# Kernel optimization log

Measured on AMD Instinct MI355X. Metric: run time of the kernel, lower is better.

The kernel has to match this reference:

```python
import jax, jax.numpy as jnp
import numpy as np

N_PITCH, N_DUR, N_TIME, N_VEL = 128, 160, 100, 128
VOCAB = N_PITCH + N_DUR + N_TIME + N_VEL  # 516
B, S = 32, 2048


def _build_vocab_tables():
    # token_type: 0='p', 1='d', 2='t', 3='v'; token_value: numeric suffix of itos_vocab[i]
    tt = np.concatenate([
        np.full(N_PITCH, 0), np.full(N_DUR, 1), np.full(N_TIME, 2), np.full(N_VEL, 3)
    ]).astype(np.int32)
    tv = np.concatenate([
        np.arange(N_PITCH), np.arange(N_DUR), np.arange(N_TIME), np.arange(N_VEL)
    ]).astype(np.float32)
    return jnp.asarray(tt), jnp.asarray(tv)


def setup_inputs() -> dict:
    key = jax.random.key(0)
    k1, k2, k3, k4 = jax.random.split(key, 4)
    token_type, token_value = _build_vocab_tables()
    return {
        "output": jax.random.normal(k1, (B, VOCAB, S), dtype=jnp.float32),
        "target": jax.random.randint(k2, (B, S), 0, VOCAB, dtype=jnp.int32),
        "token_type": token_type,
        "token_value": token_value,
        "coeff": jnp.asarray([0.5, 0.6, 0.2, 0.2], dtype=jnp.float32),
        "harmonic": jnp.asarray([0.6, 0.6, 0.2, 0.2, 0.2, 0.2, 1.5], dtype=jnp.float32),
    }


def _penalty_mask(pred, target, token_type, token_value, coeff, harmonic):
    pt, tt = token_type[pred], token_type[target]      # [B,S] type codes
    pv, tv = token_value[pred], token_value[target]    # [B,S] numeric values
    d = jnp.abs(pv - tv)
    # pitch: harmonic-interval weights (values are integer-valued floats -> exact ==)
    pitch_w = jnp.where(d == 7, harmonic[0],
              jnp.where(d == 5, harmonic[1],
              jnp.where(d == 3, harmonic[2],
              jnp.where(d == 4, harmonic[3],
              jnp.where(d == 1, harmonic[4],
              jnp.where(d == 2, harmonic[5], harmonic[6]))))))
    dur_w = coeff[1] * d / 160.0
    time_w = coeff[2] * d / 100.0
    vel_w = coeff[3] * d / 128.0
    same_type_w = jnp.where(pt == 0, pitch_w,
                  jnp.where(pt == 1, dur_w,
                  jnp.where(pt == 2, time_w, vel_w)))
    return jnp.where(pt != tt, coeff[0], same_type_w)


def reference(output, target, token_type, token_value, coeff, harmonic):
    # Faithful to original: softmax over last (seq) axis, then argmax over vocab axis 1
    sm = jax.nn.softmax(output, axis=-1)
    pred = jnp.argmax(sm, axis=1)                      # [B,S]
    # mean cross-entropy over B*S (class axis = 1)
    logp = jax.nn.log_softmax(output, axis=1)          # [B,V,S]
    nll = -jnp.take_along_axis(logp, target[:, None, :], axis=1)[:, 0, :]
    loss = nll.mean()
    mask = _penalty_mask(pred, target, token_type, token_value, coeff, harmonic)
    high_cost = (loss * mask).mean()
    return loss + high_cost
```

## Files before the change

### kernel.cpp

```cpp
#include <hip/hip_runtime.h>

#define BB 32
#define SS 2048
#define VV 516
#define NBS (BB * SS)
#define NCHUNK 16
#define NPART 256

__device__ inline float waveReduceSum(float v) {
    #pragma unroll
    for (int o = 32; o > 0; o >>= 1) v += __shfl_down(v, o, 64);
    return v;
}

__global__ __launch_bounds__(512, 4) void hl_tile(const float* __restrict__ x,
                                                  const int* __restrict__ target,
                                                  int* __restrict__ ctr,
                                                  float* __restrict__ pSum,
                                                  float* __restrict__ pBest,
                                                  int* __restrict__ pIdx,
                                                  float* __restrict__ xtArr) {
    __shared__ float ldsE[8 * 2048];
    __shared__ float sRcp[8];

    if (blockIdx.x == 0 && threadIdx.x == 0) ctr[0] = 0;

    const int c = blockIdx.x & 15, b = blockIdx.x >> 4;
    const int v0 = 32 * c + (c > 12 ? c - 12 : 0);
    const int nv = (c >= 12) ? 33 : 32;
    const int tid = threadIdx.x, lane = tid & 63, wv = tid >> 6;

    const int s0 = tid << 2;
    const int bs = b * SS + s0;
    int4 tg4 = *(const int4*)(target + bs);
    int tg[4] = {tg4.x, tg4.y, tg4.z, tg4.w};

    float sum[4], best[4], xt[4];
    int bi[4];
    #pragma unroll
    for (int i = 0; i < 4; ++i) { sum[i] = 0.f; best[i] = -1.f; bi[i] = v0; xt[i] = 0.f; }

    const float* xb = x + (size_t)(b * VV + v0) * SS;

    for (int vs = 0; vs < nv; vs += 8) {
        int m = nv - vs; if (m > 8) m = 8;
        if (wv < m) {
            const float* row = xb + (size_t)(vs + wv) * SS;
            float4 v[8];
            #pragma unroll
            for (int j = 0; j < 8; ++j)
                v[j] = *(const float4*)(row + j * 256 + lane * 4);
            float a0 = 0.f, a1 = 0.f, a2 = 0.f, a3 = 0.f;
            #pragma unroll
            for (int j = 0; j < 8; ++j) {
                float4 e;
                e.x = __expf(v[j].x); e.y = __expf(v[j].y);
                e.z = __expf(v[j].z); e.w = __expf(v[j].w);
                *(float4*)(ldsE + wv * 2048 + j * 256 + lane * 4) = e;
                a0 += e.x; a1 += e.y; a2 += e.z; a3 += e.w;
            }
            float ssum = waveReduceSum((a0 + a1) + (a2 + a3));
            if (lane == 0) sRcp[wv] = 1.f / ssum;
        }
        __syncthreads();
        for (int v = 0; v < m; ++v) {
            float r = sRcp[v];
            int vg = v0 + vs + v;
            float4 e4 = *(const float4*)(ldsE + v * 2048 + s0);
            float e[4] = {e4.x, e4.y, e4.z, e4.w};
            #pragma unroll
            for (int i = 0; i < 4; ++i) {
                sum[i] += e[i];
                float sc = e[i] * r;
                if (sc > best[i]) { best[i] = sc; bi[i] = vg; }
            }
        }
        #pragma unroll
        for (int i = 0; i < 4; ++i) {
            int lr = tg[i] - (v0 + vs);
            if (lr >= 0 && lr < m) xt[i] = __logf(ldsE[lr * 2048 + s0 + i]);
        }
        __syncthreads();
    }

    int o = c * NBS + bs;
    *(float4*)(pSum + o)  = make_float4(sum[0], sum[1], sum[2], sum[3]);
    *(float4*)(pBest + o) = make_float4(best[0], best[1], best[2], best[3]);
    *(int4*)(pIdx + o)    = make_int4(bi[0], bi[1], bi[2], bi[3]);
    int v1 = v0 + nv;
    #pragma unroll
    for (int i = 0; i < 4; ++i)
        if (tg[i] >= v0 && tg[i] < v1) xtArr[bs + i] = xt[i];
}

__global__ __launch_bounds__(256) void hl_comb(const int* __restrict__ target,
                                               const int* __restrict__ ttype,
                                               const float* __restrict__ tval,
                                               const float* __restrict__ coeff,
                                               const float* __restrict__ harm,
                                               const float* __restrict__ pSum,
                                               const float* __restrict__ pBest,
                                               const int* __restrict__ pIdx,
                                               const float* __restrict__ xtArr,
                                               float* __restrict__ pNll,
                                               float* __restrict__ pMask,
                                               int* __restrict__ counter,
                                               float* __restrict__ outv) {
    __shared__ float lds[8];
    __shared__ bool isLast;
    int idx = blockIdx.x * 256 + threadIdx.x;

    float sum = 0.f, best = -1e30f;
    int bestIdx = 0;
    #pragma unroll
    for (int c = 0; c < NCHUNK; ++c) {
        int o = c * NBS + idx;
        sum += pSum[o];
        float sc = pBest[o];
        int ii = pIdx[o];
        if (sc > best) { best = sc; bestIdx = ii; }
    }
    int tgt = target[idx];
    float nll = __logf(sum) - xtArr[idx];

    int pt = ttype[bestIdx], tt = ttype[tgt];
    float pv = tval[bestIdx], tv = tval[tgt];
    float d = fabsf(pv - tv);
    float pw = (d == 7.f) ? harm[0] : (d == 5.f) ? harm[1] : (d == 3.f) ? harm[2]
             : (d == 4.f) ? harm[3] : (d == 1.f) ? harm[4] : (d == 2.f) ? harm[5]
             : harm[6];
    float w = (pt == 0) ? pw
            : (pt == 1) ? coeff[1] * d * (1.f / 160.f)
            : (pt == 2) ? coeff[2] * d * (1.f / 100.f)
            :             coeff[3] * d * (1.f / 128.f);
    float mask = (pt != tt) ? coeff[0] : w;

    int lane = threadIdx.x & 63, wvv = threadIdx.x >> 6;
    float rn = waveReduceSum(nll);
    if (lane == 0) lds[wvv] = rn;
    __syncthreads();
    float totN = (threadIdx.x == 0) ? lds[0] + lds[1] + lds[2] + lds[3] : 0.f;
    __syncthreads();
    float rm = waveReduceSum(mask);
    if (lane == 0) lds[wvv] = rm;
    __syncthreads();
    if (threadIdx.x == 0) {
        pNll[blockIdx.x]  = totN;
        pMask[blockIdx.x] = lds[0] + lds[1] + lds[2] + lds[3];
        __threadfence();
        unsigned old = atomicAdd((unsigned*)counter, 1u);
        isLast = (old == NPART - 1);
    }
    __syncthreads();
    if (isLast) {
        __threadfence();
        int t = threadIdx.x;
        float n = waveReduceSum(pNll[t]);
        float m = waveReduceSum(pMask[t]);
        if (lane == 0) { lds[wvv] = n; lds[4 + wvv] = m; }
        __syncthreads();
        if (t == 0) {
            float tn = lds[0] + lds[1] + lds[2] + lds[3];
            float tm = lds[4] + lds[5] + lds[6] + lds[7];
            const float inv = 1.f / (float)NBS;
            outv[0] = (tn * inv) * (1.f + tm * inv);
        }
    }
}

extern "C" void kernel_launch(void* const* d_in, const int* in_sizes, int n_in,
                              void* d_out, int out_size, void* d_ws, size_t ws_size,
                              hipStream_t stream) {
    const float* x      = (const float*)d_in[0];
    const int*   target = (const int*)d_in[1];
    const int*   ttype  = (const int*)d_in[2];
    const float* tval   = (const float*)d_in[3];
    const float* coeff  = (const float*)d_in[4];
    const float* harm   = (const float*)d_in[5];

    float* ws    = (float*)d_ws;
    int*   ctr   = (int*)ws;
    float* pNll  = ws + 4;
    float* pMask = pNll + NPART;
    float* xtArr = pMask + NPART;
    float* pSum  = xtArr + NBS;
    float* pBest = pSum + (size_t)NCHUNK * NBS;
    int*   pIdx  = (int*)(pBest + (size_t)NCHUNK * NBS);

    hl_tile<<<BB * NCHUNK, 512, 0, stream>>>(x, target, ctr, pSum, pBest,
                                             pIdx, xtArr);
    hl_comb<<<NBS / 256, 256, 0, stream>>>(target, ttype, tval, coeff, harm,
                                           pSum, pBest, pIdx, xtArr,
                                           pNll, pMask, ctr, (float*)d_out);
}
```

Baseline: 46.98 us.

## Double-buffer fp16 exp tile in LDS and prefetch next row group into registers

The tile kernel now issues the global loads for the next group of 8 vocab rows right after the barrier, so they overlap with the LDS scan of the current group. The exp values are stored in LDS as fp16 across two buffers, along with double-buffered reciprocals, which removes the second barrier per iteration. The full-group case gets an unrolled scan loop. In exchange, argmax comparisons and the target log-probability now use half-precision exp values, which adds rounding error to the loss and can change argmax near ties. Register pressure also rises from the prefetched float4 buffer.

Result: faster. 44.87 us (-4.5%).

```diff
diff --git a/kernel.cpp b/kernel.cpp
--- a/kernel.cpp
+++ b/kernel.cpp
@@ -1,4 +1,5 @@
 #include <hip/hip_runtime.h>
+#include <hip/hip_fp16.h>
 
 #define BB 32
 #define SS 2048
@@ -6,6 +7,9 @@
 #define NBS (BB * SS)
 #define NCHUNK 16
 #define NPART 256
+#define BUFE (8 * 2048)
+
+struct alignas(8) h4 { __half2 a, b; };
 
 __device__ inline float waveReduceSum(float v) {
     #pragma unroll
@@ -20,67 +24,106 @@
                                                   float* __restrict__ pBest,
                                                   int* __restrict__ pIdx,
                                                   float* __restrict__ xtArr) {
-    __shared__ float ldsE[8 * 2048];
-    __shared__ float sRcp[8];
+    __shared__ __half ldsE[2 * BUFE];
+    __shared__ float sRcp[2][8];
 
     if (blockIdx.x == 0 && threadIdx.x == 0) ctr[0] = 0;
 
     const int c = blockIdx.x & 15, b = blockIdx.x >> 4;
     const int v0 = 32 * c + (c > 12 ? c - 12 : 0);
     const int nv = (c >= 12) ? 33 : 32;
+    const int nsub = (nv + 7) >> 3;
     const int tid = threadIdx.x, lane = tid & 63, wv = tid >> 6;
-
     const int s0 = tid << 2;
     const int bs = b * SS + s0;
+
     int4 tg4 = *(const int4*)(target + bs);
     int tg[4] = {tg4.x, tg4.y, tg4.z, tg4.w};
 
-    float sum[4], best[4], xt[4];
-    int bi[4];
-    #pragma unroll
-    for (int i = 0; i < 4; ++i) { sum[i] = 0.f; best[i] = -1.f; bi[i] = v0; xt[i] = 0.f; }
+    float sum[4] = {0.f, 0.f, 0.f, 0.f};
+    float best[4] = {-1.f, -1.f, -1.f, -1.f};
+    float xt[4] = {0.f, 0.f, 0.f, 0.f};
+    int bi[4] = {v0, v0, v0, v0};
 
     const float* xb = x + (size_t)(b * VV + v0) * SS;
-
-    for (int vs = 0; vs < nv; vs += 8) {
-        int m = nv - vs; if (m > 8) m = 8;
+    float4 vb[8];
+
+    {
+        const float* row = xb + (size_t)wv * SS;
+        #pragma unroll
+        for (int j = 0; j < 8; ++j)
+            vb[j] = *(const float4*)(row + j * 256 + lane * 4);
+    }
+
+    for (int k = 0; k < nsub; ++k) {
+        const int m = (nv - k * 8 < 8) ? (nv - k * 8) : 8;
+        const int kb = k & 1;
         if (wv < m) {
-            const float* row = xb + (size_t)(vs + wv) * SS;
-            float4 v[8];
-            #pragma unroll
-            for (int j = 0; j < 8; ++j)
-                v[j] = *(const float4*)(row + j * 256 + lane * 4);
+            __half* dst = ldsE + kb * BUFE + wv * 2048;
             float a0 = 0.f, a1 = 0.f, a2 = 0.f, a3 = 0.f;
             #pragma unroll
             for (int j = 0; j < 8; ++j) {
-                float4 e;
-                e.x = __expf(v[j].x); e.y = __expf(v[j].y);
-                e.z = __expf(v[j].z); e.w = __expf(v[j].w);
-                *(float4*)(ldsE + wv * 2048 + j * 256 + lane * 4) = e;
-                a0 += e.x; a1 += e.y; a2 += e.z; a3 += e.w;
+                float ex = __expf(vb[j].x), ey = __expf(vb[j].y);
+                float ez = __expf(vb[j].z), ew = __expf(vb[j].w);
+                h4 h;
+                h.a = __halves2half2(__float2half_rn(ex), __float2half_rn(ey));
+                h.b = __halves2half2(__float2half_rn(ez), __float2half_rn(ew));
+                *(h4*)(dst + j * 256 + lane * 4) = h;
+                a0 += ex; a1 += ey; a2 += ez; a3 += ew;
             }
             float ssum = waveReduceSum((a0 + a1) + (a2 + a3));
-            if (lane == 0) sRcp[wv] = 1.f / ssum;
+            if (lane == 0) sRcp[kb][wv] = 1.f / ssum;
         }
         __syncthreads();
-        for (int v = 0; v < m; ++v) {
-            float r = sRcp[v];
-            int vg = v0 + vs + v;
-            float4 e4 = *(const float4*)(ldsE + v * 2048 + s0);
-            float e[4] = {e4.x, e4.y, e4.z, e4.w};
+        if (k + 1 < nsub) {
+            int m2 = nv - (k + 1) * 8;
+            if (wv < m2) {
+                const float* row = xb + (size_t)((k + 1) * 8 + wv) * SS;
+                #pragma unroll
+                for (int j = 0; j < 8; ++j)
+                    vb[j] = *(const float4*)(row + j * 256 + lane * 4);
+            }
+        }
+        const __half* src = ldsE + kb * BUFE + s0;
+        if (m == 8) {
+            h4 r[8];
             #pragma unroll
-            for (int i = 0; i < 4; ++i) {
-                sum[i] += e[i];
-                float sc = e[i] * r;
-                if (sc > best[i]) { best[i] = sc; bi[i] = vg; }
+            for (int i = 0; i < 8; ++i)
+                r[i] = *(const h4*)(src + i * 2048);
+            #pragma unroll
+            for (int i = 0; i < 8; ++i) {
+                float rc = sRcp[kb][i];
+                int vg = v0 + k * 8 + i;
+                float e0 = __low2float(r[i].a), e1 = __high2float(r[i].a);
+                float e2 = __low2float(r[i].b), e3 = __high2float(r[i].b);
+                sum[0] += e0; sum[1] += e1; sum[2] += e2; sum[3] += e3;
+                float c0 = e0 * rc, c1 = e1 * rc, c2 = e2 * rc, c3 = e3 * rc;
+                if (c0 > best[0]) { best[0] = c0; bi[0] = vg; }
+                if (c1 > best[1]) { best[1] = c1; bi[1] = vg; }
+                if (c2 > best[2]) { best[2] = c2; bi[2] = vg; }
+                if (c3 > best[3]) { best[3] = c3; bi[3] = vg; }
+            }
+        } else {
+            for (int v = 0; v < m; ++v) {
+                h4 r = *(const h4*)(src + v * 2048);
+                float rc = sRcp[kb][v];
+                int vg = v0 + k * 8 + v;
+                float e0 = __low2float(r.a), e1 = __high2float(r.a);
+                float e2 = __low2float(r.b), e3 = __high2float(r.b);
+                sum[0] += e0; sum[1] += e1; sum[2] += e2; sum[3] += e3;
+                float c0 = e0 * rc, c1 = e1 * rc, c2 = e2 * rc, c3 = e3 * rc;
+                if (c0 > best[0]) { best[0] = c0; bi[0] = vg; }
+                if (c1 > best[1]) { best[1] = c1; bi[1] = vg; }
+                if (c2 > best[2]) { best[2] = c2; bi[2] = vg; }
+                if (c3 > best[3]) { best[3] = c3; bi[3] = vg; }
             }
         }
         #pragma unroll
         for (int i = 0; i < 4; ++i) {
-            int lr = tg[i] - (v0 + vs);
-            if (lr >= 0 && lr < m) xt[i] = __logf(ldsE[lr * 2048 + s0 + i]);
-        }
-        __syncthreads();
+            int lr = tg[i] - (v0 + k * 8);
+            if (lr >= 0 && lr < m)
+                xt[i] = __logf(__half2float(ldsE[kb * BUFE + lr * 2048 + s0 + i]));
+        }
     }
 
     int o = c * NBS + bs;
```

## Keep tile data in registers with double-buffered loads instead of LDS staging

Applied to the files above, without the earlier changes.

The tile kernel stops staging exp values through a 64KB LDS buffer. Each thread now loads its own 4 columns for 8 vocab rows straight into registers, and the next 8 rows are prefetched into a second register set while the current set is processed. Row sums are reduced across the block through a small LDS array guarded by raw barriers. The target logit is taken directly from the raw input, which removes the exp/log round trip. The cost is much higher register pressure (two float4[8] buffers per thread) and two block barriers per 8-row group.

New measurement: 145.9 us. +210.6%, slower.

```diff
diff --git a/kernel.cpp b/kernel.cpp
--- a/kernel.cpp
+++ b/kernel.cpp
@@ -7,7 +7,7 @@
 #define NCHUNK 16
 #define NPART 256
 
-__device__ inline float waveReduceSum(float v) {
+__device__ __forceinline__ float waveReduceSum(float v) {
     #pragma unroll
     for (int o = 32; o > 0; o >>= 1) v += __shfl_down(v, o, 64);
     return v;
@@ -20,7 +20,7 @@
                                                   float* __restrict__ pBest,
                                                   int* __restrict__ pIdx,
                                                   float* __restrict__ xtArr) {
-    __shared__ float ldsE[8 * 2048];
+    __shared__ float ldsR[8][8];
     __shared__ float sRcp[8];
 
     if (blockIdx.x == 0 && threadIdx.x == 0) ctr[0] = 0;
@@ -29,58 +29,111 @@
     const int v0 = 32 * c + (c > 12 ? c - 12 : 0);
     const int nv = (c >= 12) ? 33 : 32;
     const int tid = threadIdx.x, lane = tid & 63, wv = tid >> 6;
-
     const int s0 = tid << 2;
     const int bs = b * SS + s0;
+
     int4 tg4 = *(const int4*)(target + bs);
     int tg[4] = {tg4.x, tg4.y, tg4.z, tg4.w};
 
-    float sum[4], best[4], xt[4];
-    int bi[4];
-    #pragma unroll
-    for (int i = 0; i < 4; ++i) { sum[i] = 0.f; best[i] = -1.f; bi[i] = v0; xt[i] = 0.f; }
-
-    const float* xb = x + (size_t)(b * VV + v0) * SS;
-
-    for (int vs = 0; vs < nv; vs += 8) {
-        int m = nv - vs; if (m > 8) m = 8;
-        if (wv < m) {
-            const float* row = xb + (size_t)(vs + wv) * SS;
-            float4 v[8];
+    float sum[4]  = {0.f, 0.f, 0.f, 0.f};
+    float best[4] = {-1.f, -1.f, -1.f, -1.f};
+    float xt[4]   = {0.f, 0.f, 0.f, 0.f};
+    int   bi[4]   = {v0, v0, v0, v0};
+
+    const float* xb = x + (size_t)(b * VV + v0) * SS + s0;
+
+    float4 va[8], vb[8];
+    #pragma unroll
+    for (int r = 0; r < 8; ++r)
+        va[r] = *(const float4*)(xb + (size_t)r * SS);
+
+#define TILE_BODY(CUR, NXT, KK)                                               \
+    {                                                                         \
+        if ((KK) + 1 < 4) {                                                   \
+            _Pragma("unroll")                                                 \
+            for (int r = 0; r < 8; ++r)                                       \
+                NXT[r] = *(const float4*)(xb + (size_t)(((KK)+1)*8 + r) * SS);\
+        }                                                                     \
+        float rp[8];                                                          \
+        _Pragma("unroll")                                                     \
+        for (int r = 0; r < 8; ++r) {                                         \
+            int vg = v0 + (KK)*8 + r;                                         \
+            float4 xv = CUR[r];                                               \
+            if (vg == tg[0]) xt[0] = xv.x;                                    \
+            if (vg == tg[1]) xt[1] = xv.y;                                    \
+            if (vg == tg[2]) xt[2] = xv.z;                                    \
+            if (vg == tg[3]) xt[3] = xv.w;                                    \
+            float4 e;                                                         \
+            e.x = __expf(xv.x); e.y = __expf(xv.y);                           \
+            e.z = __expf(xv.z); e.w = __expf(xv.w);                           \
+            CUR[r] = e;                                                       \
+            rp[r] = (e.x + e.y) + (e.z + e.w);                                \
+        }                                                                     \
+        _Pragma("unroll")                                                     \
+        for (int r = 0; r < 8; ++r) rp[r] = waveReduceSum(rp[r]);             \
+        if (lane == 0) {                                                      \
+            _Pragma("unroll")                                                 \
+            for (int r = 0; r < 8; ++r) ldsR[wv][r] = rp[r];                  \
+        }                                                                     \
+        asm volatile("s_waitcnt lgkmcnt(0)" ::: "memory");                    \
+        __builtin_amdgcn_s_barrier();                                         \
+        if (tid < 8) {                                                        \
+            float s = 0.f;                                                    \
+            _Pragma("unroll")                                                 \
+            for (int w = 0; w < 8; ++w) s += ldsR[w][tid];                    \
+            sRcp[tid] = 1.f / s;                                              \
+        }                                                                     \
+        asm volatile("s_waitcnt lgkmcnt(0)" ::: "memory");                    \
+        __builtin_amdgcn_s_barrier();                                         \
+        _Pragma("unroll")                                                     \
+        for (int r = 0; r < 8; ++r) {                                         \
+            float rc = sRcp[r];                                               \
+            int vg = v0 + (KK)*8 + r;                                         \
+            float4 e = CUR[r];                                                \
+            sum[0] += e.x; sum[1] += e.y; sum[2] += e.z; sum[3] += e.w;       \
+            float c0 = e.x*rc, c1 = e.y*rc, c2 = e.z*rc, c3 = e.w*rc;         \
+            if (c0 > best[0]) { best[0] = c0; bi[0] = vg; }                   \
+            if (c1 > best[1]) { best[1] = c1; bi[1] = vg; }                   \
+            if (c2 > best[2]) { best[2] = c2; bi[2] = vg; }                   \
+            if (c3 > best[3]) { best[3] = c3; bi[3] = vg; }                   \
+        }                                                                     \
+    }
+
+    TILE_BODY(va, vb, 0)
+    TILE_BODY(vb, va, 1)
+    TILE_BODY(va, vb, 2)
+    TILE_BODY(vb, va, 3)
+#undef TILE_BODY
+
+    if (nv == 33) {
+        int vg = v0 + 32;
+        float4 xv = *(const float4*)(xb + (size_t)32 * SS);
+        if (vg == tg[0]) xt[0] = xv.x;
+        if (vg == tg[1]) xt[1] = xv.y;
+        if (vg == tg[2]) xt[2] = xv.z;
+        if (vg == tg[3]) xt[3] = xv.w;
+        float4 e;
+        e.x = __expf(xv.x); e.y = __expf(xv.y);
+        e.z = __expf(xv.z); e.w = __expf(xv.w);
+        float rp = waveReduceSum((e.x + e.y) + (e.z + e.w));
+        if (lane == 0) ldsR[wv][0] = rp;
+        asm volatile("s_waitcnt lgkmcnt(0)" ::: "memory");
+        __builtin_amdgcn_s_barrier();
+        if (tid == 0) {
+            float s = 0.f;
             #pragma unroll
-            for (int j = 0; j < 8; ++j)
-                v[j] = *(const float4*)(row + j * 256 + lane * 4);
-            float a0 = 0.f, a1 = 0.f, a2 = 0.f, a3 = 0.f;
-            #pragma unroll
-            for (int j = 0; j < 8; ++j) {
-                float4 e;
-                e.x = __expf(v[j].x); e.y = __expf(v[j].y);
-                e.z = __expf(v[j].z); e.w = __expf(v[j].w);
-                *(float4*)(ldsE + wv * 2048 + j * 256 + lane * 4) = e;
-                a0 += e.x; a1 += e.y; a2 += e.z; a3 += e.w;
-            }
-            float ssum = waveReduceSum((a0 + a1) + (a2 + a3));
-            if (lane == 0) sRcp[wv] = 1.f / ssum;
+            for (int w = 0; w < 8; ++w) s += ldsR[w][0];
+            sRcp[0] = 1.f / s;
         }
-        __syncthreads();
-        for (int v = 0; v < m; ++v) {
-            float r = sRcp[v];
-            int vg = v0 + vs + v;
-            float4 e4 = *(const float4*)(ldsE + v * 2048 + s0);
-            float e[4] = {e4.x, e4.y, e4.z, e4.w};
-            #pragma unroll
-            for (int i = 0; i < 4; ++i) {
-                sum[i] += e[i];
-                float sc = e[i] * r;
-                if (sc > best[i]) { best[i] = sc; bi[i] = vg; }
-            }
-        }
-        #pragma unroll
-        for (int i = 0; i < 4; ++i) {
-            int lr = tg[i] - (v0 + vs);
-            if (lr >= 0 && lr < m) xt[i] = __logf(ldsE[lr * 2048 + s0 + i]);
-        }
-        __syncthreads();
+        asm volatile("s_waitcnt lgkmcnt(0)" ::: "memory");
+        __builtin_amdgcn_s_barrier();
+        float rc = sRcp[0];
+        sum[0] += e.x; sum[1] += e.y; sum[2] += e.z; sum[3] += e.w;
+        float c0 = e.x*rc, c1 = e.y*rc, c2 = e.z*rc, c3 = e.w*rc;
+        if (c0 > best[0]) { best[0] = c0; bi[0] = vg; }
+        if (c1 > best[1]) { best[1] = c1; bi[1] = vg; }
+        if (c2 > best[2]) { best[2] = c2; bi[2] = vg; }
+        if (c3 > best[3]) { best[3] = c3; bi[3] = vg; }
     }
 
     int o = c * NBS + bs;
```

## Double-buffer fp16 exp tiles in LDS with register prefetch and single barrier

Applied to the files above, without the earlier changes.

Restructures the per-block vocab loop into eight 4-row tiles. Two waves now share each row. The next tile's global loads are prefetched into registers while the current tile is exponentiated, and exp values are written to LDS as fp16 in a double-buffered layout so only one barrier per tile is needed. The goal is to overlap HBM loads with compute and to cut LDS footprint and synchronisation. In exchange, the row sums, argmax scores and target log-probabilities are computed from half-precision exp values, which can slightly change the loss or flip near-tie argmax picks.

New measurement: 52.91 us. 1.13x slower.

```diff
diff --git a/kernel.cpp b/kernel.cpp
--- a/kernel.cpp
+++ b/kernel.cpp
@@ -1,4 +1,5 @@
 #include <hip/hip_runtime.h>
+#include <hip/hip_fp16.h>
 
 #define BB 32
 #define SS 2048
@@ -7,21 +8,23 @@
 #define NCHUNK 16
 #define NPART 256
 
-__device__ inline float waveReduceSum(float v) {
+struct alignas(8) h4 { __half2 a, b; };
+
+__device__ __forceinline__ float waveReduceSum(float v) {
     #pragma unroll
     for (int o = 32; o > 0; o >>= 1) v += __shfl_down(v, o, 64);
     return v;
 }
 
-__global__ __launch_bounds__(512, 4) void hl_tile(const float* __restrict__ x,
+__global__ __launch_bounds__(512, 2) void hl_tile(const float* __restrict__ x,
                                                   const int* __restrict__ target,
                                                   int* __restrict__ ctr,
                                                   float* __restrict__ pSum,
                                                   float* __restrict__ pBest,
                                                   int* __restrict__ pIdx,
                                                   float* __restrict__ xtArr) {
-    __shared__ float ldsE[8 * 2048];
-    __shared__ float sRcp[8];
+    __shared__ __half ldsX[2][4][2048];
+    __shared__ float  ldsH[2][4][2];
 
     if (blockIdx.x == 0 && threadIdx.x == 0) ctr[0] = 0;
 
@@ -29,59 +32,135 @@
     const int v0 = 32 * c + (c > 12 ? c - 12 : 0);
     const int nv = (c >= 12) ? 33 : 32;
     const int tid = threadIdx.x, lane = tid & 63, wv = tid >> 6;
-
+    const int row4 = wv >> 1;
+    const int half = wv & 1;
+    const int colbase = half * 1024 + lane * 4;
     const int s0 = tid << 2;
     const int bs = b * SS + s0;
+
     int4 tg4 = *(const int4*)(target + bs);
     int tg[4] = {tg4.x, tg4.y, tg4.z, tg4.w};
 
-    float sum[4], best[4], xt[4];
-    int bi[4];
-    #pragma unroll
-    for (int i = 0; i < 4; ++i) { sum[i] = 0.f; best[i] = -1.f; bi[i] = v0; xt[i] = 0.f; }
+    float sum[4]  = {0.f, 0.f, 0.f, 0.f};
+    float best[4] = {-1.f, -1.f, -1.f, -1.f};
+    float xt[4]   = {0.f, 0.f, 0.f, 0.f};
+    int   bi[4]   = {v0, v0, v0, v0};
 
     const float* xb = x + (size_t)(b * VV + v0) * SS;
 
-    for (int vs = 0; vs < nv; vs += 8) {
-        int m = nv - vs; if (m > 8) m = 8;
-        if (wv < m) {
-            const float* row = xb + (size_t)(vs + wv) * SS;
-            float4 v[8];
+    float4 vbA[4], vbB[4];
+    {
+        const float* rowp = xb + (size_t)row4 * SS + colbase;
+        #pragma unroll
+        for (int j = 0; j < 4; ++j)
+            vbA[j] = *(const float4*)(rowp + j * 256);
+    }
+
+#define TILE_BODY(CUR, NXT, KK)                                               \
+    {                                                                         \
+        if ((KK) + 1 < 8) {                                                   \
+            const float* rowp = xb + (size_t)(((KK)+1)*4 + row4) * SS + colbase;\
+            _Pragma("unroll")                                                 \
+            for (int j = 0; j < 4; ++j)                                       \
+                NXT[j] = *(const float4*)(rowp + j * 256);                    \
+        } else if (nv == 33 && wv < 2) {            \
+            const float* rowp = xb + (size_t)32 * SS + colbase;               \
+            _Pragma("unroll")                                                 \
+            for (int j = 0; j < 4; ++j)                                       \
+                NXT[j] = *(const float4*)(rowp + j * 256);                    \
+        }                                                                     \
+        {                                                     \
+            float a0 = 0.f, a1 = 0.f, a2 = 0.f, a3 = 0.f;                     \
+            __half* dst = &ldsX[(KK)&1][row4][colbase];                       \
+            _Pragma("unroll")                                                 \
+            for (int j = 0; j < 4; ++j) {                                     \
+                float ex = __expf(CUR[j].x), ey = __expf(CUR[j].y);           \
+                float ez = __expf(CUR[j].z), ew = __expf(CUR[j].w);           \
+                h4 h;                                                         \
+                h.a = __halves2half2(__float2half_rn(ex), __float2half_rn(ey));\
+                h.b = __halves2half2(__float2half_rn(ez), __float2half_rn(ew));\
+                *(h4*)(dst + j * 256) = h;                                    \
+                a0 += ex; a1 += ey; a2 += ez; a3 += ew;                       \
+            }                                                                 \
+            float rs = waveReduceSum((a0 + a1) + (a2 + a3));                  \
+            if (lane == 0) ldsH[(KK)&1][row4][half] = rs;                     \
+        }                                                                     \
+        asm volatile("s_waitcnt lgkmcnt(0)" ::: "memory");                    \
+        __builtin_amdgcn_s_barrier();                                         \
+        {                                                     \
+            h4 hv0 = *(const h4*)&ldsX[(KK)&1][0][s0];                        \
+            h4 hv1 = *(const h4*)&ldsX[(KK)&1][1][s0];                        \
+            h4 hv2 = *(const h4*)&ldsX[(KK)&1][2][s0];                        \
+            h4 hv3 = *(const h4*)&ldsX[(KK)&1][3][s0];                        \
+            float sr0 = ldsH[(KK)&1][0][0] + ldsH[(KK)&1][0][1];              \
+            float sr1 = ldsH[(KK)&1][1][0] + ldsH[(KK)&1][1][1];              \
+            float sr2 = ldsH[(KK)&1][2][0] + ldsH[(KK)&1][2][1];              \
+            float sr3 = ldsH[(KK)&1][3][0] + ldsH[(KK)&1][3][1];              \
+            ACC_ROW(hv0, sr0, v0 + (KK)*4 + 0)                                \
+            ACC_ROW(hv1, sr1, v0 + (KK)*4 + 1)                                \
+            ACC_ROW(hv2, sr2, v0 + (KK)*4 + 2)                                \
+            ACC_ROW(hv3, sr3, v0 + (KK)*4 + 3)                                \
+            _Pragma("unroll")                                                 \
+            for (int i = 0; i < 4; ++i) {                                     \
+                int lr = tg[i] - (v0 + (KK)*4);                               \
+                if (lr >= 0 && lr < 4)                                        \
+                    xt[i] = __logf(__half2float(ldsX[(KK)&1][lr][s0 + i]));   \
+            }                                                                 \
+        }                                                                     \
+    }
+
+#define ACC_ROW(HV, SR, VG)                                                   \
+    {                                                                         \
+        float rc = 1.f / (SR);                                                \
+        int vg = (VG);                                                        \
+        float e0 = __low2float((HV).a), e1 = __high2float((HV).a);            \
+        float e2 = __low2float((HV).b), e3 = __high2float((HV).b);            \
+        sum[0] += e0; sum[1] += e1; sum[2] += e2; sum[3] += e3;               \
+        float c0 = e0*rc, c1 = e1*rc, c2 = e2*rc, c3 = e3*rc;                 \
+        if (c0 > best[0]) { best[0] = c0; bi[0] = vg; }                       \
+        if (c1 > best[1]) { best[1] = c1; bi[1] = vg; }                       \
+        if (c2 > best[2]) { best[2] = c2; bi[2] = vg; }                       \
+        if (c3 > best[3]) { best[3] = c3; bi[3] = vg; }                       \
+    }
+
+    TILE_BODY(vbA, vbB, 0)
+    TILE_BODY(vbB, vbA, 1)
+    TILE_BODY(vbA, vbB, 2)
+    TILE_BODY(vbB, vbA, 3)
+    TILE_BODY(vbA, vbB, 4)
+    TILE_BODY(vbB, vbA, 5)
+    TILE_BODY(vbA, vbB, 6)
+    TILE_BODY(vbB, vbA, 7)
+#undef TILE_BODY
+
+    if (nv == 33) {
+        if (wv < 2) {
+            float a0 = 0.f, a1 = 0.f, a2 = 0.f, a3 = 0.f;
+            __half* dst = &ldsX[0][0][colbase];
             #pragma unroll
-            for (int j = 0; j < 8; ++j)
-                v[j] = *(const float4*)(row + j * 256 + lane * 4);
-            float a0 = 0.f, a1 = 0.f, a2 = 0.f, a3 = 0.f;
-            #pragma unroll
-            for (int j = 0; j < 8; ++j) {
-                float4 e;
-                e.x = __expf(v[j].x); e.y = __expf(v[j].y);
-                e.z = __expf(v[j].z); e.w = __expf(v[j].w);
-                *(float4*)(ldsE + wv * 2048 + j * 256 + lane * 4) = e;
-                a0 += e.x; a1 += e.y; a2 += e.z; a3 += e.w;
+            for (int j = 0; j < 4; ++j) {
+                float ex = __expf(vbA[j].x), ey = __expf(vbA[j].y);
+                float ez = __expf(vbA[j].z), ew = __expf(vbA[j].w);
+                h4 h;
+                h.a = __halves2half2(__float2half_rn(ex), __float2half_rn(ey));
+                h.b = __halves2half2(__float2half_rn(ez), __float2half_rn(ew));
+                *(h4*)(dst + j * 256) = h;
+                a0 += ex; a1 += ey; a2 += ez; a3 += ew;
             }
-            float ssum = waveReduceSum((a0 + a1) + (a2 + a3));
-            if (lane == 0) sRcp[wv] = 1.f / ssum;
+            float rs = waveReduceSum((a0 + a1) + (a2 + a3));
+            if (lane == 0) ldsH[0][0][half] = rs;
         }
-        __syncthreads();
-        for (int v = 0; v < m; ++v) {
-            float r = sRcp[v];
-            int vg = v0 + vs + v;
-            float4 e4 = *(const float4*)(ldsE + v * 2048 + s0);
-            float e[4] = {e4.x, e4.y, e4.z, e4.w};
-            #pragma unroll
-            for (int i = 0; i < 4; ++i) {
-                sum[i] += e[i];
-                float sc = e[i] * r;
-                if (sc > best[i]) { best[i] = sc; bi[i] = vg; }
-            }
-        }
+        asm volatile("s_waitcnt lgkmcnt(0)" ::: "memory");
+        __builtin_amdgcn_s_barrier();
+        h4 hv = *(const h4*)&ldsX[0][0][s0];
+        float sr = ldsH[0][0][0] + ldsH[0][0][1];
+        ACC_ROW(hv, sr, v0 + 32)
         #pragma unroll
-        for (int i = 0; i < 4; ++i) {
-            int lr = tg[i] - (v0 + vs);
-            if (lr >= 0 && lr < m) xt[i] = __logf(ldsE[lr * 2048 + s0 + i]);
-        }
-        __syncthreads();
-    }
+        for (int i = 0; i < 4; ++i)
+            if (tg[i] == v0 + 32)
+                xt[i] = __logf(__half2float(ldsX[0][0][s0 + i]));
+    }
+#undef ACC_ROW
 
     int o = c * NBS + bs;
     *(float4*)(pSum + o)  = make_float4(sum[0], sum[1], sum[2], sum[3]);
```
